# Performance work log

Hardware: AMD Instinct MI355X
Metric: run time of the kernel (lower is better)

The kernel has to match this reference:

```python
import jax, jax.numpy as jnp
import numpy as np

N = 4096          # total atoms
N_METAL = 1024    # first N_METAL atoms are metal (Z=79) by construction
L = 24.0          # cubic cell edge (Angstrom)
DL = 2.4
NK = 10           # int(L / DL) -- static k-grid extent per axis
SIGMA = 1.0 / 1.805132
SCALING = 1.0
FOUR_PI = 4.0 * np.pi

# static integer reciprocal grid with k=0 removed: (K,3), K = (2*NK+1)^3 - 1
_g = np.arange(-NK, NK + 1)
_INTS = np.stack(np.meshgrid(_g, _g, _g, indexing="ij"), axis=-1).reshape(-1, 3)
_INTS = _INTS[np.any(_INTS != 0, axis=1)].astype(np.float32)


def _ewald_potential(r, q, cell):
    """Reciprocal-space Ewald potential at each atom position.
    r: (n,3) positions, q: (n,m) charges (m charge columns), cell: (3,3)
    rows = lattice vectors. Returns (n,m) potential ('field' f in cace).
    pot_i = (4*pi/V) * sum_k exp(-sigma^2 k^2/2)/k^2 * Re[S(k) e^{-ik.r_i}]."""
    recip = (2.0 * np.pi) * jnp.linalg.inv(cell).T      # rows b1,b2,b3
    k = jnp.asarray(_INTS, dtype=r.dtype) @ recip       # (K,3)
    k2 = jnp.sum(k * k, axis=1)                         # (K,)
    kfac = jnp.exp((-0.5 * SIGMA * SIGMA) * k2) / k2    # (K,)
    vol = jnp.abs(jnp.linalg.det(cell))
    kr = r @ k.T                                        # (n,K)  dominant alloc
    c, s = jnp.cos(kr), jnp.sin(kr)
    sf_c = c.T @ q                                      # (K,m) structure factors
    sf_s = s.T @ q
    pot = c @ (kfac[:, None] * sf_c) + s @ (kfac[:, None] * sf_s)
    return (FOUR_PI / vol) * pot


def setup_inputs() -> dict:
    key = jax.random.key(0)
    k1, k2 = jax.random.split(key)
    positions = jax.random.uniform(k1, (N, 3), dtype=jnp.float32) * L
    q = jax.random.normal(k2, (N, 1), dtype=jnp.float32) * 0.1
    cell = (L * jnp.eye(3, dtype=jnp.float32)).reshape(1, 3, 3)
    atomic_numbers = jnp.concatenate([
        jnp.full((N_METAL,), 79, dtype=jnp.int32),   # metal block first
        jnp.full((N - N_METAL,), 8, dtype=jnp.int32),
    ])
    batch = jnp.zeros((N,), dtype=jnp.int32)         # single system
    return {"positions": positions, "q": q, "cell": cell,
            "atomic_numbers": atomic_numbers, "batch": batch}


def reference(positions, q, cell, atomic_numbers, batch):
    # single batch (batch all zeros); metal atoms are the first N_METAL
    # (atomic_numbers == 79 by construction, so the boolean mask is static)
    cell0 = cell.reshape(3, 3)
    q = q.at[:N_METAL].set(0.0)                      # q_all[metal] = 0
    r_m = positions[:N_METAL]

    # _compute_S_matrix: pairwise Ewald kernel among metal atoms via q=eye
    A = _ewald_potential(r_m, jnp.eye(N_METAL, dtype=positions.dtype), cell0)
    coeffs = jnp.ones((N_METAL + 1, N_METAL + 1), dtype=positions.dtype)
    coeffs = coeffs.at[:N_METAL, :N_METAL].set(A)
    coeffs = coeffs.at[N_METAL, N_METAL].set(0.0)
    S = jnp.linalg.inv(coeffs)                       # cached AJl in torch code

    # field at every atom from all (electrolyte) charges
    f = _ewald_potential(positions, q, cell0)        # (N,1)

    # external_field is None -> B_ext = 0, no external energy
    B = -f[:N_METAL] * SCALING                       # (N_METAL,1)
    chi = jnp.concatenate([B, jnp.zeros((1, 1), dtype=B.dtype)], axis=0)
    sol = S @ chi                                    # (N_METAL+1,1)
    q_mw = q.at[:N_METAL].set(sol[:-1] / SCALING)
    return q_mw
```

## Files before the change

### kernel.cpp

```cpp
#include <hip/hip_runtime.h>
#include <math.h>

#define NATOM 4096
#define NM    1024
#define NKR   9260
#define KSPLIT 14
#define CHPS  22
#define NCH   308
#define KC    32
#define KPAD2 9856
#define PI_F  3.14159265358979f

typedef short v8s __attribute__((ext_vector_type(8)));
typedef float v4f __attribute__((ext_vector_type(4)));

static __device__ __forceinline__ void kdata(int t, const float* __restrict__ cell,
                                             float& kxx, float& kyy, float& kzz, float& w) {
  if (t >= NKR) { kxx = 0.f; kyy = 0.f; kzz = 0.f; w = 0.f; return; }
  int u = (t < 4630) ? t : t + 1;
  int a = u / 441;
  int rem = u - a * 441;
  int b = rem / 21;
  int c = rem - b * 21;
  float na = (float)(a - 10), nb = (float)(b - 10), nc = (float)(c - 10);
  float m00=cell[0], m01=cell[1], m02=cell[2];
  float m10=cell[3], m11=cell[4], m12=cell[5];
  float m20=cell[6], m21=cell[7], m22=cell[8];
  float det = m00*(m11*m22 - m12*m21) - m01*(m10*m22 - m12*m20) + m02*(m10*m21 - m11*m20);
  float inv00 =  (m11*m22 - m12*m21) / det;
  float inv01 = -(m01*m22 - m02*m21) / det;
  float inv02 =  (m01*m12 - m02*m11) / det;
  float inv10 = -(m10*m22 - m12*m20) / det;
  float inv11 =  (m00*m22 - m02*m20) / det;
  float inv12 = -(m00*m12 - m02*m10) / det;
  float inv20 =  (m10*m21 - m11*m20) / det;
  float inv21 = -(m00*m21 - m01*m20) / det;
  float inv22 =  (m00*m11 - m01*m10) / det;
  const float twopi = 2.f * PI_F;
  kxx = twopi * (na*inv00 + nb*inv01 + nc*inv02);
  kyy = twopi * (na*inv10 + nb*inv11 + nc*inv12);
  kzz = twopi * (na*inv20 + nb*inv21 + nc*inv22);
  float k2 = kxx*kxx + kyy*kyy + kzz*kzz;
  const float sigma = 1.0f / 1.805132f;
  w = (4.f * PI_F / fabsf(det)) * __expf(-0.5f * sigma * sigma * k2) / k2;
}

__global__ __launch_bounds__(256)
void sfk(const float* __restrict__ pos, const float* __restrict__ q,
         const float* __restrict__ cell,
         float* __restrict__ kx, float* __restrict__ ky,
         float* __restrict__ kz, float* __restrict__ ksw,
         float* __restrict__ gc, float* __restrict__ gs) {
  __shared__ float red1[8][32], red2[8][32];
  const int kloc = threadIdx.x & 31;
  const int part = threadIdx.x >> 5;
  const int k = blockIdx.x * 32 + kloc;
  float kxx, kyy, kzz, w;
  kdata(k, cell, kxx, kyy, kzz, w);
  if (part == 0) { kx[k]=kxx; ky[k]=kyy; kz[k]=kzz; ksw[k]=sqrtf(w); }
  float sc = 0.f, ss = 0.f;
  const int j0 = NM + part * 384, j1 = j0 + 384;
  for (int j = j0; j < j1; ++j) {
    float kr = kxx*pos[3*j] + kyy*pos[3*j+1] + kzz*pos[3*j+2];
    float s, c;
    __sincosf(kr, &s, &c);
    float qj = q[j];
    sc += qj * c;
    ss += qj * s;
  }
  red1[part][kloc] = sc;
  red2[part][kloc] = ss;
  __syncthreads();
  if (part == 0) {
    float tc = 0.f, ts = 0.f;
    #pragma unroll
    for (int pp = 0; pp < 8; ++pp) { tc += red1[pp][kloc]; ts += red2[pp][kloc]; }
    gc[k] = w * tc;
    gs[k] = w * ts;
  }
}

__global__ __launch_bounds__(256)
void fB(const float* __restrict__ pos,
        const float* __restrict__ kx, const float* __restrict__ ky,
        const float* __restrict__ kz,
        const float* __restrict__ gc, const float* __restrict__ gs,
        float* __restrict__ r1, float* __restrict__ r2) {
  int i = blockIdx.x;
  float px = pos[3*i], py = pos[3*i+1], pz = pos[3*i+2];
  float p = 0.f;
  for (int k = threadIdx.x; k < KPAD2; k += 256) {
    float kr = kx[k]*px + ky[k]*py + kz[k]*pz;
    float s, c;
    __sincosf(kr, &s, &c);
    p += gc[k]*c + gs[k]*s;
  }
  for (int o = 32; o > 0; o >>= 1) p += __shfl_down(p, o, 64);
  __shared__ float red[4];
  if ((threadIdx.x & 63) == 0) red[threadIdx.x >> 6] = p;
  __syncthreads();
  if (threadIdx.x == 0) {
    r1[i] = -(red[0] + red[1] + red[2] + red[3]);
    r2[i] = 1.f;
  }
}

#define PSTR 40
__global__ __launch_bounds__(256, 2)
void gemmA(const float* __restrict__ pos,
           const float* __restrict__ kx, const float* __restrict__ ky,
           const float* __restrict__ kz, const float* __restrict__ ksw,
           float* __restrict__ A) {
  __shared__ short Pl[8][128 * PSTR];
  const int blk = blockIdx.x;
  const int split = blk / 36;
  const int tt = blk - split * 36;
  int bi = 0, rem = tt;
  while (rem >= 8 - bi) { rem -= 8 - bi; ++bi; }
  const int bj = bi + rem;
  const int t = threadIdx.x;
  const int side = t >> 7;
  const int a = t & 127;
  const int atom = (side ? bj : bi) * 128 + a;
  const float px = pos[3*atom], py = pos[3*atom+1], pz = pos[3*atom+2];
  short* PC_hi = &Pl[side*4+0][a*PSTR];
  short* PC_mi = &Pl[side*4+1][a*PSTR];
  short* PS_hi = &Pl[side*4+2][a*PSTR];
  short* PS_mi = &Pl[side*4+3][a*PSTR];

  const int w = t >> 6;
  const int lane = t & 63;
  const int ln15 = lane & 15;
  const int quad = lane >> 4;

  v4f acc[2][8];
  #pragma unroll
  for (int mt = 0; mt < 2; ++mt)
    #pragma unroll
    for (int nt = 0; nt < 8; ++nt) {
      v4f z = {0.f, 0.f, 0.f, 0.f};
      acc[mt][nt] = z;
    }

  for (int ch = split * CHPS; ch < split * CHPS + CHPS; ++ch) {
    const int kb = ch * KC;
    #pragma unroll
    for (int g = 0; g < 4; ++g) {
      v8s vch, vcm, vsh, vsm;
      #pragma unroll
      for (int j = 0; j < 8; ++j) {
        const int gk = kb + g*8 + j;
        float kr = kx[gk]*px + ky[gk]*py + kz[gk]*pz;
        float s, c;
        __sincosf(kr, &s, &c);
        float sw = ksw[gk];
        float cv = c * sw, sv = s * sw;
        unsigned cu = __float_as_uint(cv);
        float chf = __uint_as_float(cu & 0xffff0000u);
        unsigned cmu = __float_as_uint(cv - chf);
        unsigned su = __float_as_uint(sv);
        float shf = __uint_as_float(su & 0xffff0000u);
        unsigned smu = __float_as_uint(sv - shf);
        vch[j] = (short)(cu >> 16);
        vcm[j] = (short)(cmu >> 16);
        vsh[j] = (short)(su >> 16);
        vsm[j] = (short)(smu >> 16);
      }
      *(v8s*)&PC_hi[g*8] = vch;
      *(v8s*)&PC_mi[g*8] = vcm;
      *(v8s*)&PS_hi[g*8] = vsh;
      *(v8s*)&PS_mi[g*8] = vsm;
    }
    __syncthreads();
    v8s aCh[2], aCm[2], aSh[2], aSm[2];
    #pragma unroll
    for (int mt = 0; mt < 2; ++mt) {
      const int off = (w*32 + mt*16 + ln15) * PSTR + quad*8;
      aCh[mt] = *(const v8s*)&Pl[0][off];
      aCm[mt] = *(const v8s*)&Pl[1][off];
      aSh[mt] = *(const v8s*)&Pl[2][off];
      aSm[mt] = *(const v8s*)&Pl[3][off];
    }
    #pragma unroll
    for (int nt = 0; nt < 8; ++nt) {
      const int off = (nt*16 + ln15) * PSTR + quad*8;
      v8s bCh = *(const v8s*)&Pl[4][off];
      v8s bCm = *(const v8s*)&Pl[5][off];
      v8s bSh = *(const v8s*)&Pl[6][off];
      v8s bSm = *(const v8s*)&Pl[7][off];
      #pragma unroll
      for (int mt = 0; mt < 2; ++mt) {
        v4f d = acc[mt][nt];
        d = __builtin_amdgcn_mfma_f32_16x16x32_bf16(aCh[mt], bCh, d, 0, 0, 0);
        d = __builtin_amdgcn_mfma_f32_16x16x32_bf16(aCh[mt], bCm, d, 0, 0, 0);
        d = __builtin_amdgcn_mfma_f32_16x16x32_bf16(aCm[mt], bCh, d, 0, 0, 0);
        d = __builtin_amdgcn_mfma_f32_16x16x32_bf16(aSh[mt], bSh, d, 0, 0, 0);
        d = __builtin_amdgcn_mfma_f32_16x16x32_bf16(aSh[mt], bSm, d, 0, 0, 0);
        d = __builtin_amdgcn_mfma_f32_16x16x32_bf16(aSm[mt], bSh, d, 0, 0, 0);
        acc[mt][nt] = d;
      }
    }
    __syncthreads();
  }
  #pragma unroll
  for (int mt = 0; mt < 2; ++mt)
    #pragma unroll
    for (int nt = 0; nt < 8; ++nt)
      #pragma unroll
      for (int r = 0; r < 4; ++r) {
        const int row = bi*128 + w*32 + mt*16 + quad*4 + r;
        const int col = bj*128 + nt*16 + ln15;
        atomicAdd(&A[row*1024 + col], acc[mt][nt][r]);
      }
}

__global__ __launch_bounds__(256)
void step(float* __restrict__ A, const float* __restrict__ r1, const float* __restrict__ r2,
          float* __restrict__ ru1, float* __restrict__ ru2,
          float* __restrict__ y1g, float* __restrict__ y2g, int p) {
  __shared__ float D[32][33];
  __shared__ float T[32][33];
  __shared__ float y1s[32], y2s[32];
  const int t = threadIdx.x;
  const int nb = 32 - p;
  const int i0 = (t >> 4) * 2, j0 = (t & 15) * 2;

  if ((int)blockIdx.x >= nb) {
    int rem = blockIdx.x - nb, a = 0;
    while (rem >= a + 1) { rem -= (a + 1); ++a; }
    const int qi = p + 1 + a, qj = p + 1 + rem;
    for (int e = t; e < 1024; e += 256) {
      int r = e >> 5, c = e & 31;
      D[r][c] = A[(qi*32+r)*1024 + (p-1)*32 + c];
      T[r][c] = A[(qj*32+r)*1024 + (p-1)*32 + c];
    }
    float o[2][2];
    if (p == 1 && (qi >> 2) != (qj >> 2)) {
      #pragma unroll
      for (int ii = 0; ii < 2; ++ii)
        #pragma unroll
        for (int jj = 0; jj < 2; ++jj)
          o[ii][jj] = A[(qj*32 + j0+jj)*1024 + qi*32 + i0+ii];
    } else {
      #pragma unroll
      for (int ii = 0; ii < 2; ++ii)
        #pragma unroll
        for (int jj = 0; jj < 2; ++jj)
          o[ii][jj] = A[(qi*32+i0+ii)*1024 + qj*32 + j0+jj];
    }
    __syncthreads();
    for (int m = 0; m < 32; ++m) {
      float a0 = D[i0+0][m], a1 = D[i0+1][m];
      float b0 = T[j0+0][m], b1 = T[j0+1][m];
      o[0][0]-=a0*b0; o[0][1]-=a0*b1;
      o[1][0]-=a1*b0; o[1][1]-=a1*b1;
    }
    #pragma unroll
    for (int ii = 0; ii < 2; ++ii)
      #pragma unroll
      for (int jj = 0; jj < 2; ++jj)
        A[(qi*32+i0+ii)*1024 + qj*32 + j0+jj] = o[ii][jj];
    return;
  }

  const int b = blockIdx.x;
  const int q = p + b;
  if (p == 0) {
    for (int e = t; e < 1024; e += 256)
      D[e>>5][e&31] = A[(e>>5)*1024 + (e&31)];
    if (b > 0) {
      if (q < 4) {
        for (int e = t; e < 1024; e += 256)
          T[e>>5][e&31] = A[(q*32+(e>>5))*1024 + (e&31)];
      } else {
        for (int e = t; e < 1024; e += 256)
          T[e&31][e>>5] = A[(e>>5)*1024 + q*32 + (e&31)];
      }
    }
    __syncthreads();
  } else {
    for (int e = t; e < 1024; e += 256)
      D[e>>5][e&31] = A[(p*32+(e>>5))*1024 + (p-1)*32 + (e&31)];
    if (b > 0)
      for (int e = t; e < 1024; e += 256)
        T[e>>5][e&31] = A[(q*32+(e>>5))*1024 + (p-1)*32 + (e&31)];
    __syncthreads();
    float o1[2][2];
    #pragma unroll
    for (int ii = 0; ii < 2; ++ii)
      #pragma unroll
      for (int jj = 0; jj < 2; ++jj)
        o1[ii][jj] = A[(p*32+i0+ii)*1024 + p*32 + j0+jj];
    for (int m = 0; m < 32; ++m) {
      float a0 = D[i0+0][m], a1 = D[i0+1][m];
      float b0 = D[j0+0][m], b1 = D[j0+1][m];
      o1[0][0]-=a0*b0; o1[0][1]-=a0*b1;
      o1[1][0]-=a1*b0; o1[1][1]-=a1*b1;
    }
    float o2[2][2];
    if (b > 0) {
      if (p == 1 && (q >> 2) != 0) {
        #pragma unroll
        for (int ii = 0; ii < 2; ++ii)
          #pragma unroll
          for (int jj = 0; jj < 2; ++jj)
            o2[ii][jj] = A[(1*32 + j0+jj)*1024 + q*32 + i0+ii];
      } else {
        #pragma unroll
        for (int ii = 0; ii < 2; ++ii)
          #pragma unroll
          for (int jj = 0; jj < 2; ++jj)
            o2[ii][jj] = A[(q*32+i0+ii)*1024 + p*32 + j0+jj];
      }
      for (int m = 0; m < 32; ++m) {
        float a0 = T[i0+0][m], a1 = T[i0+1][m];
        float b0 = D[j0+0][m], b1 = D[j0+1][m];
        o2[0][0]-=a0*b0; o2[0][1]-=a0*b1;
        o2[1][0]-=a1*b0; o2[1][1]-=a1*b1;
      }
    }
    __syncthreads();
    #pragma unroll
    for (int ii = 0; ii < 2; ++ii)
      #pragma unroll
      for (int jj = 0; jj < 2; ++jj)
        D[i0+ii][j0+jj] = o1[ii][jj];
    if (b > 0) {
      #pragma unroll
      for (int ii = 0; ii < 2; ++ii)
        #pragma unroll
        for (int jj = 0; jj < 2; ++jj)
          T[i0+ii][j0+jj] = o2[ii][jj];
    }
    __syncthreads();
  }

  if (t < 32) {
    float a[32];
    #pragma unroll
    for (int m = 0; m < 32; ++m) a[m] = D[t][m];
    #pragma unroll
    for (int j = 0; j < 32; ++j) {
      float dj = __shfl(a[j], j);
      float rinv = rsqrtf(dj);
      float lj = (t == j) ? dj * rinv : a[j] * rinv;
      a[j] = lj;
      #pragma unroll
      for (int m = j + 1; m < 32; ++m)
        a[m] -= lj * __shfl(lj, m);
    }
    #pragma unroll
    for (int m = 0; m < 32; ++m) D[t][m] = a[m];
  }
  __syncthreads();
  if (b == 0) {
    for (int e = t; e < 1024; e += 256) {
      int i = e >> 5, j = e & 31;
      if (i >= j) A[(p*32+i)*1024 + p*32 + j] = D[i][j];
    }
  } else {
    if (t < 32) {
      #pragma unroll
      for (int cb = 0; cb < 2; ++cb) {
        const int cbase = cb * 16;
        float x[16];
        #pragma unroll
        for (int k = 0; k < 16; ++k) x[k] = T[t][cbase + k];
        for (int m = 0; m < cbase; ++m) {
          float tm = T[t][m];
          #pragma unroll
          for (int k = 0; k < 16; ++k)
            x[k] -= tm * D[cbase + k][m];
        }
        #pragma unroll
        for (int k = 0; k < 16; ++k) {
          float xv = x[k] * (1.0f / D[cbase + k][cbase + k]);
          x[k] = xv;
          #pragma unroll
          for (int m2 = k + 1; m2 < 16; ++m2)
            x[m2] -= xv * D[cbase + m2][cbase + k];
        }
        #pragma unroll
        for (int k = 0; k < 16; ++k) T[t][cbase + k] = x[k];
      }
    }
    __syncthreads();
    for (int e = t; e < 1024; e += 256)
      A[(q*32 + (e>>5))*1024 + p*32 + (e&31)] = T[e>>5][e&31];
  }
  __syncthreads();
  if (t < 32) {
    float v1 = r1[p*32 + t], v2 = r2[p*32 + t];
    for (int j = 0; j < 32; ++j) {
      float invd = 1.f / D[j][j];
      float Lij = D[t][j];
      float x1 = __shfl(v1, j) * invd;
      float x2 = __shfl(v2, j) * invd;
      if (t == j)      { v1 = x1; v2 = x2; }
      else if (t > j)  { v1 -= Lij * x1; v2 -= Lij * x2; }
    }
    y1s[t] = v1; y2s[t] = v2;
    if (b == 0) { y1g[p*32 + t] = v1; y2g[p*32 + t] = v2; }
  }
  __syncthreads();
  if (b > 0 && t < 32) {
    float a1 = 0.f, a2 = 0.f;
    for (int j = 0; j < 32; ++j) {
      float lv = T[t][j];
      a1 += lv * y1s[j];
      a2 += lv * y2s[j];
    }
    ru1[q*32 + t] -= a1;
    ru2[q*32 + t] -= a2;
  }
}

__global__ __launch_bounds__(256)
void bwd_solve(const float* __restrict__ A, float* __restrict__ y1g, float* __restrict__ y2g,
               const float* __restrict__ qin, float* __restrict__ out, int S, int finalize) {
  __shared__ float D[64][65];
  __shared__ float x1s[64], x2s[64];
  __shared__ float rs1[4], rs2[4];
  const int t = threadIdx.x;
  const int base0 = S * 256;
  for (int j3 = 3; j3 >= 0; --j3) {
    const int base = base0 + j3 * 64;
    for (int e = t; e < 4096; e += 256)
      D[e>>6][e&63] = A[(base + (e>>6))*1024 + base + (e&63)];
    __syncthreads();
    if (t < 64) {
      float v1 = y1g[base + t], v2 = y2g[base + t];
      for (int i = 63; i >= 0; --i) {
        float invd = 1.f / D[i][i];
        float x1 = __shfl(v1, i) * invd;
        float x2 = __shfl(v2, i) * invd;
        float Lim = D[i][t];
        if (t == i)      { v1 = x1; v2 = x2; }
        else if (t < i)  { v1 -= Lim * x1; v2 -= Lim * x2; }
      }
      y1g[base + t] = v1; y2g[base + t] = v2;
      x1s[t] = v1; x2s[t] = v2;
    }
    __syncthreads();
    const int nup = j3 * 64;
    for (int rr = t; rr < nup; rr += 256) {
      float a1 = 0.f, a2 = 0.f;
      #pragma unroll 8
      for (int jj = 0; jj < 64; ++jj) {
        float lv = A[(base+jj)*1024 + base0 + rr];
        a1 += lv * x1s[jj];
        a2 += lv * x2s[jj];
      }
      y1g[base0+rr] -= a1; y2g[base0+rr] -= a2;
    }
    __syncthreads();
  }
  if (finalize) {
    float s1 = 0.f, s2 = 0.f;
    for (int e = t; e < 1024; e += 256) { s1 += y1g[e]; s2 += y2g[e]; }
    for (int o = 32; o > 0; o >>= 1) { s1 += __shfl_down(s1, o, 64); s2 += __shfl_down(s2, o, 64); }
    if ((t & 63) == 0) { rs1[t >> 6] = s1; rs2[t >> 6] = s2; }
    __syncthreads();
    const float lam = (rs1[0]+rs1[1]+rs1[2]+rs1[3]) / (rs2[0]+rs2[1]+rs2[2]+rs2[3]);
    for (int e = t; e < 1024; e += 256) out[e] = y1g[e] - lam * y2g[e];
    for (int e = NM + t; e < NATOM; e += 256) out[e] = qin[e];
  }
}

__global__ __launch_bounds__(256)
void bwd_upd(const float* __restrict__ A, float* __restrict__ y1g, float* __restrict__ y2g, int S) {
  __shared__ float x1s[256], x2s[256];
  __shared__ float p1[4][64], p2[4][64];
  const int t = threadIdx.x;
  const int rbase = blockIdx.x * 64;
  const int r = t & 63;
  const int slice = t >> 6;
  x1s[t] = y1g[S*256 + t];
  x2s[t] = y2g[S*256 + t];
  __syncthreads();
  float a1 = 0.f, a2 = 0.f;
  for (int j = slice*64; j < slice*64 + 64; ++j) {
    float lv = A[(S*256 + j)*1024 + rbase + r];
    a1 += lv * x1s[j];
    a2 += lv * x2s[j];
  }
  p1[slice][r] = a1; p2[slice][r] = a2;
  __syncthreads();
  if (t < 64) {
    y1g[rbase + t] -= p1[0][t] + p1[1][t] + p1[2][t] + p1[3][t];
    y2g[rbase + t] -= p2[0][t] + p2[1][t] + p2[2][t] + p2[3][t];
  }
}

extern "C" void kernel_launch(void* const* d_in, const int* in_sizes, int n_in,
                              void* d_out, int out_size, void* d_ws, size_t ws_size,
                              hipStream_t stream) {
  const float* pos  = (const float*)d_in[0];
  const float* q    = (const float*)d_in[1];
  const float* cell = (const float*)d_in[2];
  float* out = (float*)d_out;

  float* ws  = (float*)d_ws;
  float* A   = ws;
  float* kx  = ws + 1048576;
  float* ky  = kx + KPAD2;
  float* kz  = ky + KPAD2;
  float* ksw = kz + KPAD2;
  float* gc  = ksw + KPAD2;
  float* gs  = gc + KPAD2;
  float* r1  = gs + KPAD2;
  float* r2  = r1 + 1024;
  float* y1g = r2 + 1024;
  float* y2g = y1g + 1024;

  sfk<<<NCH, 256, 0, stream>>>(pos, q, cell, kx, ky, kz, ksw, gc, gs);
  fB<<<NM, 256, 0, stream>>>(pos, kx, ky, kz, gc, gs, r1, r2);
  hipMemsetAsync(A, 0, 1024 * 1024 * sizeof(float), stream);
  gemmA<<<36 * KSPLIT, 256, 0, stream>>>(pos, kx, ky, kz, ksw, A);
  for (int p = 0; p < 32; ++p) {
    const int s = 31 - p;
    const int grid = (32 - p) + ((p >= 1) ? s * (s + 1) / 2 : 0);
    step<<<grid, 256, 0, stream>>>(A, r1, r2, r1, r2, y1g, y2g, p);
  }
  for (int S = 3; S >= 0; --S) {
    bwd_solve<<<1, 256, 0, stream>>>(A, y1g, y2g, q, out, S, S == 0);
    if (S > 0) bwd_upd<<<4 * S, 256, 0, stream>>>(A, y1g, y2g, S);
  }
}
```

Before: 979.7 us.

## Process two Cholesky panel columns per launch with separate L buffer

Restructures the blocked Cholesky factorization to handle two 32-wide panel columns per kernel launch, halving the number of sequential step launches from 32 to 16. The factor is now written to a separate L matrix so trailing updates from the previous pair can be applied lazily while the current diagonal and panel tiles are recomputed. Launch count and serialization overhead drop, but each block does redundant factorization work (several blocks recompute the same diagonal Cholesky and TRSM), and shared memory use grows to eleven tiles.

```diff
diff --git a/kernel.cpp b/kernel.cpp
--- a/kernel.cpp
+++ b/kernel.cpp
@@ -214,28 +214,119 @@
       }
 }
 
+static __device__ __forceinline__ void ldTile(float (*B)[33], const float* __restrict__ M,
+                                              int rt, int ct, int t) {
+  for (int e = t; e < 1024; e += 256)
+    B[e>>5][e&31] = M[(rt*32 + (e>>5))*1024 + ct*32 + (e&31)];
+}
+static __device__ __forceinline__ void ldTileT(float (*B)[33], const float* __restrict__ M,
+                                               int rt, int ct, int t) {
+  for (int e = t; e < 1024; e += 256)
+    B[e&31][e>>5] = M[(ct*32 + (e>>5))*1024 + rt*32 + (e&31)];
+}
+static __device__ __forceinline__ void ldPanelTile(float (*B)[33], const float* __restrict__ A,
+                                                   int q, int pc, int t) {
+  if (pc >= 4 || q < 4) ldTile(B, A, q, pc, t);
+  else ldTileT(B, A, q, pc, t);
+}
+static __device__ __forceinline__ void ranksub(float (*O)[33], float (*X)[33], float (*Y)[33], int t) {
+  const int i0 = (t >> 4) * 2, j0 = (t & 15) * 2;
+  float o00=O[i0][j0], o01=O[i0][j0+1], o10=O[i0+1][j0], o11=O[i0+1][j0+1];
+  for (int m = 0; m < 32; ++m) {
+    float a0 = X[i0][m], a1 = X[i0+1][m];
+    float b0 = Y[j0][m], b1 = Y[j0+1][m];
+    o00-=a0*b0; o01-=a0*b1; o10-=a1*b0; o11-=a1*b1;
+  }
+  O[i0][j0]=o00; O[i0][j0+1]=o01; O[i0+1][j0]=o10; O[i0+1][j0+1]=o11;
+}
+static __device__ __forceinline__ void chol32(float (*D)[33], int t) {
+  if (t < 32) {
+    float a[32];
+    #pragma unroll
+    for (int m = 0; m < 32; ++m) a[m] = D[t][m];
+    #pragma unroll
+    for (int j = 0; j < 32; ++j) {
+      float dj = __shfl(a[j], j);
+      float rinv = rsqrtf(dj);
+      float lj = (t == j) ? dj * rinv : a[j] * rinv;
+      a[j] = lj;
+      #pragma unroll
+      for (int m = j + 1; m < 32; ++m) a[m] -= lj * __shfl(lj, m);
+    }
+    #pragma unroll
+    for (int m = 0; m < 32; ++m) D[t][m] = a[m];
+  }
+}
+static __device__ __forceinline__ void trsm32(float (*T)[33], float (*D)[33], int t) {
+  if (t < 32) {
+    #pragma unroll
+    for (int cb = 0; cb < 2; ++cb) {
+      const int cbase = cb * 16;
+      float x[16];
+      #pragma unroll
+      for (int k = 0; k < 16; ++k) x[k] = T[t][cbase + k];
+      for (int m = 0; m < cbase; ++m) {
+        float tm = T[t][m];
+        #pragma unroll
+        for (int k = 0; k < 16; ++k) x[k] -= tm * D[cbase + k][m];
+      }
+      #pragma unroll
+      for (int k = 0; k < 16; ++k) {
+        float xv = x[k] * (1.0f / D[cbase + k][cbase + k]);
+        x[k] = xv;
+        #pragma unroll
+        for (int m2 = k + 1; m2 < 16; ++m2) x[m2] -= xv * D[cbase + m2][cbase + k];
+      }
+      #pragma unroll
+      for (int k = 0; k < 16; ++k) T[t][cbase + k] = x[k];
+    }
+  }
+}
+static __device__ __forceinline__ void fwd32(float (*D)[33], float& v1, float& v2, int t) {
+  for (int j = 0; j < 32; ++j) {
+    float invd = 1.f / D[j][j];
+    float Lij = D[t][j];
+    float x1 = __shfl(v1, j) * invd;
+    float x2 = __shfl(v2, j) * invd;
+    if (t == j)      { v1 = x1; v2 = x2; }
+    else if (t > j)  { v1 -= Lij * x1; v2 -= Lij * x2; }
+  }
+}
+static __device__ __forceinline__ void stTileFull(float* __restrict__ L, float (*B)[33],
+                                                  int rt, int ct, int t) {
+  for (int e = t; e < 1024; e += 256)
+    L[(rt*32 + (e>>5))*1024 + ct*32 + (e&31)] = B[e>>5][e&31];
+}
+static __device__ __forceinline__ void stTileLow(float* __restrict__ L, float (*B)[33],
+                                                 int rt, int ct, int t) {
+  for (int e = t; e < 1024; e += 256) {
+    int i = e>>5, j = e&31;
+    if (i >= j) L[(rt*32 + i)*1024 + ct*32 + j] = B[i][j];
+  }
+}
+
 __global__ __launch_bounds__(256)
-void step(float* __restrict__ A, const float* __restrict__ r1, const float* __restrict__ r2,
-          float* __restrict__ ru1, float* __restrict__ ru2,
-          float* __restrict__ y1g, float* __restrict__ y2g, int p) {
-  __shared__ float D[32][33];
-  __shared__ float T[32][33];
-  __shared__ float y1s[32], y2s[32];
+void step2(float* __restrict__ A, float* __restrict__ L,
+           float* __restrict__ r1, float* __restrict__ r2,
+           float* __restrict__ y1g, float* __restrict__ y2g, int P) {
+  __shared__ float DA[32][33], DB[32][33], RB[32][33], OWN[32][33], LQ[32][33];
+  __shared__ float Z0[32][33], Z1[32][33], W0[32][33], W1[32][33], V0[32][33], V1[32][33];
+  __shared__ float ya1[32], ya2[32], yb1[32], yb2[32];
   const int t = threadIdx.x;
-  const int nb = 32 - p;
+  const int p0 = 2*P, p1 = p0 + 1;
+  const int z0 = p0 - 2, z1 = p0 - 1;
+  const int nbA = 32 - p0, nbB = 31 - p0;
+  const int b = blockIdx.x;
   const int i0 = (t >> 4) * 2, j0 = (t & 15) * 2;
 
-  if ((int)blockIdx.x >= nb) {
-    int rem = blockIdx.x - nb, a = 0;
+  if (b >= nbA + nbB) {
+    int rem = b - (nbA + nbB), a = 0;
     while (rem >= a + 1) { rem -= (a + 1); ++a; }
-    const int qi = p + 1 + a, qj = p + 1 + rem;
-    for (int e = t; e < 1024; e += 256) {
-      int r = e >> 5, c = e & 31;
-      D[r][c] = A[(qi*32+r)*1024 + (p-1)*32 + c];
-      T[r][c] = A[(qj*32+r)*1024 + (p-1)*32 + c];
-    }
+    const int qi = p0 + 2 + a, qj = p0 + 2 + rem;
+    ldTile(Z0, L, qi, z0, t); ldTile(Z1, L, qi, z1, t);
+    ldTile(W0, L, qj, z0, t); ldTile(W1, L, qj, z1, t);
     float o[2][2];
-    if (p == 1 && (qi >> 2) != (qj >> 2)) {
+    if (P == 1 && (qi >> 2) != (qj >> 2)) {
       #pragma unroll
       for (int ii = 0; ii < 2; ++ii)
         #pragma unroll
@@ -250,10 +341,14 @@
     }
     __syncthreads();
     for (int m = 0; m < 32; ++m) {
-      float a0 = D[i0+0][m], a1 = D[i0+1][m];
-      float b0 = T[j0+0][m], b1 = T[j0+1][m];
-      o[0][0]-=a0*b0; o[0][1]-=a0*b1;
-      o[1][0]-=a1*b0; o[1][1]-=a1*b1;
+      float a0 = Z0[i0][m], a1 = Z0[i0+1][m];
+      float b0 = W0[j0][m], b1 = W0[j0+1][m];
+      o[0][0]-=a0*b0; o[0][1]-=a0*b1; o[1][0]-=a1*b0; o[1][1]-=a1*b1;
+    }
+    for (int m = 0; m < 32; ++m) {
+      float a0 = Z1[i0][m], a1 = Z1[i0+1][m];
+      float b0 = W1[j0][m], b1 = W1[j0+1][m];
+      o[0][0]-=a0*b0; o[0][1]-=a0*b1; o[1][0]-=a1*b0; o[1][1]-=a1*b1;
     }
     #pragma unroll
     for (int ii = 0; ii < 2; ++ii)
@@ -263,160 +358,108 @@
     return;
   }
 
-  const int b = blockIdx.x;
-  const int q = p + b;
-  if (p == 0) {
-    for (int e = t; e < 1024; e += 256)
-      D[e>>5][e&31] = A[(e>>5)*1024 + (e&31)];
+  if (b < nbA) {
+    const int q = p0 + b;
+    ldTile(DA, A, p0, p0, t);
+    if (P >= 1) { ldTile(Z0, L, p0, z0, t); ldTile(Z1, L, p0, z1, t); }
     if (b > 0) {
-      if (q < 4) {
-        for (int e = t; e < 1024; e += 256)
-          T[e>>5][e&31] = A[(q*32+(e>>5))*1024 + (e&31)];
-      } else {
-        for (int e = t; e < 1024; e += 256)
-          T[e&31][e>>5] = A[(e>>5)*1024 + q*32 + (e&31)];
-      }
-    }
-    __syncthreads();
-  } else {
-    for (int e = t; e < 1024; e += 256)
-      D[e>>5][e&31] = A[(p*32+(e>>5))*1024 + (p-1)*32 + (e&31)];
-    if (b > 0)
-      for (int e = t; e < 1024; e += 256)
-        T[e>>5][e&31] = A[(q*32+(e>>5))*1024 + (p-1)*32 + (e&31)];
-    __syncthreads();
-    float o1[2][2];
-    #pragma unroll
-    for (int ii = 0; ii < 2; ++ii)
-      #pragma unroll
-      for (int jj = 0; jj < 2; ++jj)
-        o1[ii][jj] = A[(p*32+i0+ii)*1024 + p*32 + j0+jj];
-    for (int m = 0; m < 32; ++m) {
-      float a0 = D[i0+0][m], a1 = D[i0+1][m];
-      float b0 = D[j0+0][m], b1 = D[j0+1][m];
-      o1[0][0]-=a0*b0; o1[0][1]-=a0*b1;
-      o1[1][0]-=a1*b0; o1[1][1]-=a1*b1;
-    }
-    float o2[2][2];
-    if (b > 0) {
-      if (p == 1 && (q >> 2) != 0) {
-        #pragma unroll
-        for (int ii = 0; ii < 2; ++ii)
-          #pragma unroll
-          for (int jj = 0; jj < 2; ++jj)
-            o2[ii][jj] = A[(1*32 + j0+jj)*1024 + q*32 + i0+ii];
-      } else {
-        #pragma unroll
-        for (int ii = 0; ii < 2; ++ii)
-          #pragma unroll
-          for (int jj = 0; jj < 2; ++jj)
-            o2[ii][jj] = A[(q*32+i0+ii)*1024 + p*32 + j0+jj];
-      }
-      for (int m = 0; m < 32; ++m) {
-        float a0 = T[i0+0][m], a1 = T[i0+1][m];
-        float b0 = D[j0+0][m], b1 = D[j0+1][m];
-        o2[0][0]-=a0*b0; o2[0][1]-=a0*b1;
-        o2[1][0]-=a1*b0; o2[1][1]-=a1*b1;
-      }
-    }
-    __syncthreads();
-    #pragma unroll
-    for (int ii = 0; ii < 2; ++ii)
-      #pragma unroll
-      for (int jj = 0; jj < 2; ++jj)
-        D[i0+ii][j0+jj] = o1[ii][jj];
-    if (b > 0) {
-      #pragma unroll
-      for (int ii = 0; ii < 2; ++ii)
-        #pragma unroll
-        for (int jj = 0; jj < 2; ++jj)
-          T[i0+ii][j0+jj] = o2[ii][jj];
-    }
-    __syncthreads();
-  }
-
+      ldPanelTile(OWN, A, q, p0, t);
+      if (P >= 1) { ldTile(W0, L, q, z0, t); ldTile(W1, L, q, z1, t); }
+    }
+    __syncthreads();
+    if (P >= 1) {
+      ranksub(DA, Z0, Z0, t);
+      ranksub(DA, Z1, Z1, t);
+      if (b > 0) { ranksub(OWN, W0, Z0, t); ranksub(OWN, W1, Z1, t); }
+      __syncthreads();
+    }
+    chol32(DA, t);
+    __syncthreads();
+    if (b == 0) {
+      stTileLow(L, DA, p0, p0, t);
+      if (t < 32) {
+        float v1 = r1[p0*32 + t], v2 = r2[p0*32 + t];
+        fwd32(DA, v1, v2, t);
+        y1g[p0*32 + t] = v1; y2g[p0*32 + t] = v2;
+      }
+    } else {
+      trsm32(OWN, DA, t);
+      __syncthreads();
+      stTileFull(L, OWN, q, p0, t);
+    }
+    return;
+  }
+
+  const int bb = b - nbA;
+  const int q = p1 + bb;
+  ldTile(DA, A, p0, p0, t);
+  ldTile(DB, A, p1, p1, t);
+  ldPanelTile(RB, A, p1, p0, t);
+  if (P >= 1) {
+    ldTile(Z0, L, p0, z0, t); ldTile(Z1, L, p0, z1, t);
+    ldTile(W0, L, p1, z0, t); ldTile(W1, L, p1, z1, t);
+  }
+  __syncthreads();
+  if (P >= 1) {
+    ranksub(DA, Z0, Z0, t); ranksub(DA, Z1, Z1, t);
+    ranksub(RB, W0, Z0, t); ranksub(RB, W1, Z1, t);
+    ranksub(DB, W0, W0, t); ranksub(DB, W1, W1, t);
+    __syncthreads();
+  }
+  chol32(DA, t);
+  __syncthreads();
+  trsm32(RB, DA, t);
+  __syncthreads();
+  ranksub(DB, RB, RB, t);
+  __syncthreads();
+  chol32(DB, t);
+  __syncthreads();
   if (t < 32) {
-    float a[32];
-    #pragma unroll
-    for (int m = 0; m < 32; ++m) a[m] = D[t][m];
-    #pragma unroll
-    for (int j = 0; j < 32; ++j) {
-      float dj = __shfl(a[j], j);
-      float rinv = rsqrtf(dj);
-      float lj = (t == j) ? dj * rinv : a[j] * rinv;
-      a[j] = lj;
-      #pragma unroll
-      for (int m = j + 1; m < 32; ++m)
-        a[m] -= lj * __shfl(lj, m);
-    }
-    #pragma unroll
-    for (int m = 0; m < 32; ++m) D[t][m] = a[m];
-  }
-  __syncthreads();
-  if (b == 0) {
-    for (int e = t; e < 1024; e += 256) {
-      int i = e >> 5, j = e & 31;
-      if (i >= j) A[(p*32+i)*1024 + p*32 + j] = D[i][j];
-    }
-  } else {
-    if (t < 32) {
-      #pragma unroll
-      for (int cb = 0; cb < 2; ++cb) {
-        const int cbase = cb * 16;
-        float x[16];
-        #pragma unroll
-        for (int k = 0; k < 16; ++k) x[k] = T[t][cbase + k];
-        for (int m = 0; m < cbase; ++m) {
-          float tm = T[t][m];
-          #pragma unroll
-          for (int k = 0; k < 16; ++k)
-            x[k] -= tm * D[cbase + k][m];
-        }
-        #pragma unroll
-        for (int k = 0; k < 16; ++k) {
-          float xv = x[k] * (1.0f / D[cbase + k][cbase + k]);
-          x[k] = xv;
-          #pragma unroll
-          for (int m2 = k + 1; m2 < 16; ++m2)
-            x[m2] -= xv * D[cbase + m2][cbase + k];
-        }
-        #pragma unroll
-        for (int k = 0; k < 16; ++k) T[t][cbase + k] = x[k];
-      }
-    }
-    __syncthreads();
-    for (int e = t; e < 1024; e += 256)
-      A[(q*32 + (e>>5))*1024 + p*32 + (e&31)] = T[e>>5][e&31];
+    float v1 = r1[p0*32 + t], v2 = r2[p0*32 + t];
+    fwd32(DA, v1, v2, t);
+    ya1[t] = v1; ya2[t] = v2;
   }
   __syncthreads();
   if (t < 32) {
-    float v1 = r1[p*32 + t], v2 = r2[p*32 + t];
-    for (int j = 0; j < 32; ++j) {
-      float invd = 1.f / D[j][j];
-      float Lij = D[t][j];
-      float x1 = __shfl(v1, j) * invd;
-      float x2 = __shfl(v2, j) * invd;
-      if (t == j)      { v1 = x1; v2 = x2; }
-      else if (t > j)  { v1 -= Lij * x1; v2 -= Lij * x2; }
-    }
-    y1s[t] = v1; y2s[t] = v2;
-    if (b == 0) { y1g[p*32 + t] = v1; y2g[p*32 + t] = v2; }
-  }
-  __syncthreads();
-  if (b > 0 && t < 32) {
+    float u1 = r1[p1*32 + t], u2 = r2[p1*32 + t];
+    for (int j = 0; j < 32; ++j) { float lv = RB[t][j]; u1 -= lv * ya1[j]; u2 -= lv * ya2[j]; }
+    fwd32(DB, u1, u2, t);
+    if (bb == 0) { y1g[p1*32 + t] = u1; y2g[p1*32 + t] = u2; }
+    yb1[t] = u1; yb2[t] = u2;
+  }
+  __syncthreads();
+  if (bb == 0) {
+    stTileLow(L, DB, p1, p1, t);
+    return;
+  }
+  ldPanelTile(OWN, A, q, p1, t);
+  ldPanelTile(LQ,  A, q, p0, t);
+  if (P >= 1) { ldTile(V0, L, q, z0, t); ldTile(V1, L, q, z1, t); }
+  __syncthreads();
+  if (P >= 1) {
+    ranksub(LQ,  V0, Z0, t);  ranksub(LQ,  V1, Z1, t);
+    ranksub(OWN, V0, W0, t);  ranksub(OWN, V1, W1, t);
+    __syncthreads();
+  }
+  trsm32(LQ, DA, t);
+  __syncthreads();
+  ranksub(OWN, LQ, RB, t);
+  __syncthreads();
+  trsm32(OWN, DB, t);
+  __syncthreads();
+  stTileFull(L, OWN, q, p1, t);
+  if (t < 32) {
     float a1 = 0.f, a2 = 0.f;
-    for (int j = 0; j < 32; ++j) {
-      float lv = T[t][j];
-      a1 += lv * y1s[j];
-      a2 += lv * y2s[j];
-    }
-    ru1[q*32 + t] -= a1;
-    ru2[q*32 + t] -= a2;
+    for (int j = 0; j < 32; ++j) { float lv = LQ[t][j]; a1 += lv * ya1[j]; a2 += lv * ya2[j]; }
+    float c1 = 0.f, c2 = 0.f;
+    for (int j = 0; j < 32; ++j) { float lv = OWN[t][j]; c1 += lv * yb1[j]; c2 += lv * yb2[j]; }
+    r1[q*32 + t] -= a1; r1[q*32 + t] -= c1;
+    r2[q*32 + t] -= a2; r2[q*32 + t] -= c2;
   }
 }
 
 __global__ __launch_bounds__(256)
-void bwd_solve(const float* __restrict__ A, float* __restrict__ y1g, float* __restrict__ y2g,
+void bwd_solve(const float* __restrict__ L, float* __restrict__ y1g, float* __restrict__ y2g,
                const float* __restrict__ qin, float* __restrict__ out, int S, int finalize) {
   __shared__ float D[64][65];
   __shared__ float x1s[64], x2s[64];
@@ -426,7 +469,7 @@
   for (int j3 = 3; j3 >= 0; --j3) {
     const int base = base0 + j3 * 64;
     for (int e = t; e < 4096; e += 256)
-      D[e>>6][e&63] = A[(base + (e>>6))*1024 + base + (e&63)];
+      D[e>>6][e&63] = L[(base + (e>>6))*1024 + base + (e&63)];
     __syncthreads();
     if (t < 64) {
       float v1 = y1g[base + t], v2 = y2g[base + t];
@@ -447,7 +490,7 @@
       float a1 = 0.f, a2 = 0.f;
       #pragma unroll 8
       for (int jj = 0; jj < 64; ++jj) {
-        float lv = A[(base+jj)*1024 + base0 + rr];
+        float lv = L[(base+jj)*1024 + base0 + rr];
         a1 += lv * x1s[jj];
         a2 += lv * x2s[jj];
       }
@@ -468,7 +511,7 @@
 }
 
 __global__ __launch_bounds__(256)
-void bwd_upd(const float* __restrict__ A, float* __restrict__ y1g, float* __restrict__ y2g, int S) {
+void bwd_upd(const float* __restrict__ L, float* __restrict__ y1g, float* __restrict__ y2g, int S) {
   __shared__ float x1s[256], x2s[256];
   __shared__ float p1[4][64], p2[4][64];
   const int t = threadIdx.x;
@@ -480,7 +523,7 @@
   __syncthreads();
   float a1 = 0.f, a2 = 0.f;
   for (int j = slice*64; j < slice*64 + 64; ++j) {
-    float lv = A[(S*256 + j)*1024 + rbase + r];
+    float lv = L[(S*256 + j)*1024 + rbase + r];
     a1 += lv * x1s[j];
     a2 += lv * x2s[j];
   }
@@ -502,7 +545,8 @@
 
   float* ws  = (float*)d_ws;
   float* A   = ws;
-  float* kx  = ws + 1048576;
+  float* Lm  = ws + 1048576;
+  float* kx  = Lm + 1048576;
   float* ky  = kx + KPAD2;
   float* kz  = ky + KPAD2;
   float* ksw = kz + KPAD2;
@@ -517,13 +561,13 @@
   fB<<<NM, 256, 0, stream>>>(pos, kx, ky, kz, gc, gs, r1, r2);
   hipMemsetAsync(A, 0, 1024 * 1024 * sizeof(float), stream);
   gemmA<<<36 * KSPLIT, 256, 0, stream>>>(pos, kx, ky, kz, ksw, A);
-  for (int p = 0; p < 32; ++p) {
-    const int s = 31 - p;
-    const int grid = (32 - p) + ((p >= 1) ? s * (s + 1) / 2 : 0);
-    step<<<grid, 256, 0, stream>>>(A, r1, r2, r1, r2, y1g, y2g, p);
+  for (int P = 0; P < 16; ++P) {
+    const int s = 30 - 2*P;
+    const int grid = (63 - 4*P) + ((P >= 1) ? s * (s + 1) / 2 : 0);
+    step2<<<grid, 256, 0, stream>>>(A, Lm, r1, r2, y1g, y2g, P);
   }
   for (int S = 3; S >= 0; --S) {
-    bwd_solve<<<1, 256, 0, stream>>>(A, y1g, y2g, q, out, S, S == 0);
-    if (S > 0) bwd_upd<<<4 * S, 256, 0, stream>>>(A, y1g, y2g, S);
-  }
-}
+    bwd_solve<<<1, 256, 0, stream>>>(Lm, y1g, y2g, q, out, S, S == 0);
+    if (S > 0) bwd_upd<<<4 * S, 256, 0, stream>>>(Lm, y1g, y2g, S);
+  }
+}
```

New measurement: 1.226 ms. +25.1%, slower.
